# Kernel optimization log

Measured on AMD Instinct MI355X. Metric: run time of the kernel, lower is better.

## Reference

```python
import jax, jax.numpy as jnp
import numpy as np

LOC_SIZE, LOC_EMB = 100000, 256
TIM_SIZE, TIM_EMB = 48, 64
UID_SIZE, UID_EMB = 5000, 128
HID = 512
B, T = 64, 128
L_HIST, G = 1024, 4  # 256 history groups of size 4


def setup_inputs() -> dict:
    key = jax.random.key(0)
    ks = jax.random.split(key, 16)
    s = 0.02
    inp = {
        "loc": jax.random.randint(ks[0], (B, T), 0, LOC_SIZE),
        "tim": jax.random.randint(ks[1], (B, T), 0, TIM_SIZE),
        "input_lengths": jax.random.randint(ks[2], (B,), 1, T + 1),
        "history_loc": jax.random.randint(ks[3], (B, L_HIST), 0, LOC_SIZE),
        "history_tim": jax.random.randint(ks[4], (B, L_HIST), 0, TIM_SIZE),
        "history_uid": jax.random.randint(ks[5], (B, L_HIST), 0, UID_SIZE),
        "group_size": G,
        "emb_loc": jax.random.normal(ks[6], (LOC_SIZE, LOC_EMB), jnp.float32) * s,
        "emb_tim": jax.random.normal(ks[7], (TIM_SIZE, TIM_EMB), jnp.float32) * s,
        "emb_uid": jax.random.normal(ks[8], (UID_SIZE, UID_EMB), jnp.float32) * s,
        "W_attn": jax.random.normal(ks[9], (HID, LOC_EMB + TIM_EMB + UID_EMB), jnp.float32) * s,
        "b_attn": jnp.zeros((HID,), jnp.float32),
        "W_ih": jax.random.normal(ks[10], (3 * HID, LOC_EMB + TIM_EMB), jnp.float32) * s,
        "b_ih": jnp.zeros((3 * HID,), jnp.float32),
        "W_hh": jax.random.normal(ks[11], (3 * HID, HID), jnp.float32) * s,
        "b_hh": jnp.zeros((3 * HID,), jnp.float32),
        "W_final": jax.random.normal(ks[12], (UID_SIZE, 3 * HID), jnp.float32) * s,
        "b_final": jnp.zeros((UID_SIZE,), jnp.float32),
    }
    return inp


def _gru(x_seq, W_ih, b_ih, W_hh, b_hh):
    # x_seq: [T, B, Din] -> outputs [T, B, H], PyTorch gate order (r, z, n)
    H = W_hh.shape[1]
    gx = jnp.einsum("tbd,gd->tbg", x_seq, W_ih) + b_ih  # [T,B,3H]
    h0 = jnp.zeros((x_seq.shape[1], H), x_seq.dtype)

    def step(h, gx_t):
        gh = h @ W_hh.T + b_hh
        xr, xz, xn = jnp.split(gx_t, 3, axis=-1)
        hr, hz, hn = jnp.split(gh, 3, axis=-1)
        r = jax.nn.sigmoid(xr + hr)
        z = jax.nn.sigmoid(xz + hz)
        n = jnp.tanh(xn + r * hn)
        h_new = (1.0 - z) * n + z * h
        return h_new, h_new

    _, outs = jax.lax.scan(step, h0, gx)
    return outs  # [T,B,H]


def reference(loc, tim, input_lengths, history_loc, history_tim, history_uid,
              group_size, emb_loc, emb_tim, emb_uid, W_attn, b_attn,
              W_ih, b_ih, W_hh, b_hh, W_final, b_final):
    Bn, Tn = loc.shape
    # current-trajectory embeddings -> GRU (dropout is identity in eval)
    x = jnp.concatenate([emb_loc[loc], emb_tim[tim]], axis=-1)  # [B,T,Din]
    outs = _gru(jnp.swapaxes(x, 0, 1), W_ih, b_ih, W_hh, b_hh)  # [T,B,H]
    outs = jnp.swapaxes(outs, 0, 1)                              # [B,T,H]
    last = outs[jnp.arange(Bn), input_lengths - 1]               # [B,H]

    # history pooling: groups of size G; uid emb averaged within group,
    # loc/tim embeddings taken at each group's first element
    Gc = group_size
    n_groups = history_uid.shape[1] // Gc
    uid_h = emb_uid[history_uid].reshape(Bn, n_groups, Gc, -1).mean(axis=2)  # [B,N,Du]
    loc_h = emb_loc[history_loc[:, ::Gc]]                                    # [B,N,Dl]
    tim_h = emb_tim[history_tim[:, ::Gc]]                                    # [B,N,Dt]
    hist = jnp.concatenate([loc_h, tim_h, uid_h], axis=-1)
    hist = jnp.tanh(jnp.einsum("bnd,hd->bnh", hist, W_attn) + b_attn)        # [B,N,H]

    # 'dot' attention: replaces the nested python-loop scoring
    energies = jnp.einsum("bh,bnh->bn", last, hist)
    attn_w = jax.nn.softmax(energies, axis=-1)
    context = jnp.einsum("bn,bnh->bh", attn_w, hist)

    out = jnp.concatenate([last, context, last], axis=-1)  # [B,3H]
    y = out @ W_final.T + b_final                          # [B,U]
    # original assigns y (one row) into score[t] of shape [T,U] -> broadcast over T
    score = jnp.broadcast_to(y[:, None, :], (Bn, Tn, y.shape[-1]))
    return score
```

## Files before the change

kernel.cpp:

```cpp
#include <hip/hip_runtime.h>
#include <hip/hip_bf16.h>


typedef __attribute__((ext_vector_type(8))) short bf16x8;
typedef __attribute__((ext_vector_type(4))) float f32x4;
typedef __attribute__((ext_vector_type(4))) unsigned short u16x4;
typedef __attribute__((ext_vector_type(2))) unsigned long long u64x2;
typedef unsigned long long u64;

__device__ inline unsigned short f2bf(float x) {
  __hip_bfloat16 b = __float2bfloat16(x);
  return __builtin_bit_cast(unsigned short, b);
}
__device__ inline bf16x8 pack8(float4 a, float4 b) {
  bf16x8 w;
  w[0]=(short)f2bf(a.x); w[1]=(short)f2bf(a.y); w[2]=(short)f2bf(a.z); w[3]=(short)f2bf(a.w);
  w[4]=(short)f2bf(b.x); w[5]=(short)f2bf(b.y); w[6]=(short)f2bf(b.z); w[7]=(short)f2bf(b.w);
  return w;
}

__global__ __launch_bounds__(256)
void gemm_gx_f(const int* __restrict__ loc, const int* __restrict__ tim,
               const float* __restrict__ eloc, const float* __restrict__ etim,
               const float* __restrict__ W_ih, const float* __restrict__ b_ih,
               float* __restrict__ gx) {
  constexpr int LDR = 40, K = 320, N = 1536;
  __shared__ short Asl[128 * LDR];
  __shared__ short Bsl[128 * LDR];
  const int tid = threadIdx.x;
  const int lane = tid & 63, wid = tid >> 6;
  const int wr = wid >> 1, wc = wid & 1;
  const int m16 = lane & 15, g4 = lane >> 4;
  const int bm = blockIdx.y * 128, bn = blockIdx.x * 128;
  const int srow = tid >> 1, shalf = tid & 1;
  f32x4 acc[4][4] = {};
  for (int k0 = 0; k0 < K; k0 += 32) {
    {
      const int grow = bm + srow;
      const int t = grow >> 6, b = grow & 63;
      const float* ap = (k0 < 256)
        ? eloc + (size_t)loc[b * 128 + t] * 256 + k0 + (shalf << 4)
        : etim + (size_t)tim[b * 128 + t] * 64 + (k0 - 256) + (shalf << 4);
      float4 f0 = ((const float4*)ap)[0], f1 = ((const float4*)ap)[1];
      float4 f2 = ((const float4*)ap)[2], f3 = ((const float4*)ap)[3];
      short* arow = Asl + srow * LDR + (shalf << 4);
      *(bf16x8*)(arow)     = pack8(f0, f1);
      *(bf16x8*)(arow + 8) = pack8(f2, f3);
      const float* bp = W_ih + (size_t)(bn + srow) * K + k0 + (shalf << 4);
      f0 = ((const float4*)bp)[0]; f1 = ((const float4*)bp)[1];
      f2 = ((const float4*)bp)[2]; f3 = ((const float4*)bp)[3];
      short* brow = Bsl + srow * LDR + (shalf << 4);
      *(bf16x8*)(brow)     = pack8(f0, f1);
      *(bf16x8*)(brow + 8) = pack8(f2, f3);
    }
    __syncthreads();
    bf16x8 af[4], bfr[4];
#pragma unroll
    for (int i = 0; i < 4; ++i) {
      af[i]  = *(const bf16x8*)(Asl + ((wr << 6) + (i << 4) + m16) * LDR + (g4 << 3));
      bfr[i] = *(const bf16x8*)(Bsl + ((wc << 6) + (i << 4) + m16) * LDR + (g4 << 3));
    }
#pragma unroll
    for (int i = 0; i < 4; ++i)
#pragma unroll
      for (int j = 0; j < 4; ++j)
        acc[i][j] = __builtin_amdgcn_mfma_f32_16x16x32_bf16(af[i], bfr[j], acc[i][j], 0, 0, 0);
    __syncthreads();
  }
#pragma unroll
  for (int i = 0; i < 4; ++i)
#pragma unroll
    for (int j = 0; j < 4; ++j) {
      const int col = bn + (wc << 6) + (j << 4) + m16;
      const float bv = b_ih[col];
#pragma unroll
      for (int q = 0; q < 4; ++q) {
        const int row = bm + (wr << 6) + (i << 4) + (g4 << 2) + q;
        gx[(size_t)row * N + col] = acc[i][j][q] + bv;
      }
    }
}

__global__ __launch_bounds__(256)
void gru_attn(const float* __restrict__ gx, const float* __restrict__ W_hh,
              const float* __restrict__ b_hh, const int* __restrict__ lens,
              short* __restrict__ h_bf, float* __restrict__ lastb,
              unsigned int* __restrict__ flags,
              const int* __restrict__ hloc, const int* __restrict__ htim,
              const int* __restrict__ huid,
              const float* __restrict__ eloc, const float* __restrict__ etim,
              const float* __restrict__ euid,
              const float* __restrict__ W_attn, const float* __restrict__ b_attn,
              float* __restrict__ histt) {
  __shared__ short smem[6 * 16 * 512];
  const int bid = blockIdx.x;
  const int tid = threadIdx.x;

  if (bid < 64) {
    if (tid >= 128) {
      for (int t = 0; t < 128; ++t) __syncthreads();
      return;
    }
    const int lane = tid & 63, tt = tid >> 6;
    const int c = bid >> 2, grp = bid & 3;
    const int j0 = (c << 5) + (tt << 4);
    const int b0 = grp << 4;
    const int m16 = lane & 15, g4 = lane >> 4;

    for (int gi = 0; gi < 3; ++gi) {
      const float* wg = W_hh + (size_t)(gi * 512 + j0) * 512;
      short* slab = smem + (((gi << 1) + tt) << 13);
      for (int r = 0; r < 16; ++r) {
        int k = lane << 3;
        const float4* src = (const float4*)(wg + (size_t)r * 512 + k);
        int off = ((r << 9) + k) ^ ((r & 7) << 3);
        *(bf16x8*)(slab + off) = pack8(src[0], src[1]);
      }
    }
    __syncthreads();

    const int bcol = b0 + m16;
    const int jr = j0 + (g4 << 2);
    const f32x4 bhr = *(const f32x4*)&b_hh[jr];
    const f32x4 bhz = *(const f32x4*)&b_hh[512 + jr];
    const f32x4 bhn = *(const f32x4*)&b_hh[1024 + jr];
    const int lenb = lens[bcol];
    f32x4 hprev = {0.f, 0.f, 0.f, 0.f};

    unsigned int* gflags = flags + (grp << 8);
    unsigned int* ownflag = gflags + (c << 4);

    for (int t = 0; t < 128; ++t) {
      const float* gxb = gx + ((size_t)t * 64 + bcol) * 1536;
      f32x4 gr = *(const f32x4*)(gxb + jr);
      f32x4 gz = *(const f32x4*)(gxb + 512 + jr);
      f32x4 gn = *(const f32x4*)(gxb + 1024 + jr);
      f32x4 ar = {0.f, 0.f, 0.f, 0.f}, az = ar, an = ar;
      if (t) {
        unsigned tgt = (unsigned)t;
        while (true) {
          unsigned f = tgt;
          if (lane < 16)
            f = __hip_atomic_load(gflags + (lane << 4), __ATOMIC_RELAXED, __HIP_MEMORY_SCOPE_AGENT);
          if (__all((int)(f >= tgt))) break;
        }
        asm volatile("" ::: "memory");

        const u64* hp = (const u64*)(h_bf + ((t & 1) << 15) + (size_t)bcol * 512 + (g4 << 3));
        u64 hu[32];
#pragma unroll
        for (int ks = 0; ks < 16; ++ks) {
          hu[2 * ks]     = __hip_atomic_load(hp + ks * 8,     __ATOMIC_RELAXED, __HIP_MEMORY_SCOPE_AGENT);
          hu[2 * ks + 1] = __hip_atomic_load(hp + ks * 8 + 1, __ATOMIC_RELAXED, __HIP_MEMORY_SCOPE_AGENT);
        }
#define GRU_MFMA(ks)                                                                 \
        {                                                                            \
          u64x2 p; p[0] = hu[2 * (ks)]; p[1] = hu[2 * (ks) + 1];                     \
          bf16x8 hf = __builtin_bit_cast(bf16x8, p);                                 \
          int off = ((m16 << 9) + ((ks) << 5) + (g4 << 3)) ^ ((m16 & 7) << 3);       \
          ar = __builtin_amdgcn_mfma_f32_16x16x32_bf16(*(const bf16x8*)(smem + ((0 + tt) << 13) + off), hf, ar, 0, 0, 0); \
          az = __builtin_amdgcn_mfma_f32_16x16x32_bf16(*(const bf16x8*)(smem + ((2 + tt) << 13) + off), hf, az, 0, 0, 0); \
          an = __builtin_amdgcn_mfma_f32_16x16x32_bf16(*(const bf16x8*)(smem + ((4 + tt) << 13) + off), hf, an, 0, 0, 0); \
        }
        GRU_MFMA(0)  GRU_MFMA(1)  GRU_MFMA(2)  GRU_MFMA(3)
        GRU_MFMA(4)  GRU_MFMA(5)  GRU_MFMA(6)  GRU_MFMA(7)
        GRU_MFMA(8)  GRU_MFMA(9)  GRU_MFMA(10) GRU_MFMA(11)
        GRU_MFMA(12) GRU_MFMA(13) GRU_MFMA(14) GRU_MFMA(15)
#undef GRU_MFMA
      }
      u16x4 hw;
#pragma unroll
      for (int q = 0; q < 4; ++q) {
        float r = 1.f / (1.f + __expf(-(gr[q] + ar[q] + bhr[q])));
        float z = 1.f / (1.f + __expf(-(gz[q] + az[q] + bhz[q])));
        float xn = gn[q] + r * (an[q] + bhn[q]);
        float n = 1.f - 2.f / (__expf(2.f * xn) + 1.f);
        float hv = (1.f - z) * n + z * hprev[q];
        hprev[q] = hv;
        hw[q] = f2bf(hv);
      }
      __hip_atomic_store((u64*)(h_bf + ((~t & 1) << 15) + (size_t)bcol * 512 + jr),
                         __builtin_bit_cast(u64, hw),
                         __ATOMIC_RELAXED, __HIP_MEMORY_SCOPE_AGENT);
      if (t == lenb - 1) {
        *(f32x4*)(lastb + (size_t)bcol * 512 + jr) = hprev;
      }
      if (t < 127) {
        asm volatile("s_waitcnt vmcnt(0)" ::: "memory");
        __syncthreads();
        if (tid == 0)
          __hip_atomic_store(ownflag, (unsigned)(t + 1), __ATOMIC_RELAXED, __HIP_MEMORY_SCOPE_AGENT);
      }
    }
    return;
  }

  constexpr int LDR = 40, K = 448, N = 512;
  short* Asl = smem;
  short* Bsl = smem + 128 * LDR;
  const int lane = tid & 63, wid = tid >> 6;
  const int wr = wid >> 1, wc = wid & 1;
  const int m16 = lane & 15, g4 = lane >> 4;
  const int srow = tid >> 1, shalf = tid & 1;
  for (int tile = bid - 64; tile < 512; tile += 128) {
    const int yt = tile >> 2, nt = tile & 3;
    const int bm = yt << 7, bn = nt << 7;
    f32x4 acc[4][4] = {};
    for (int k0 = 0; k0 < K; k0 += 32) {
      {
        const int grow = bm + srow;
        const int b = grow >> 8, n = grow & 255;
        const int base = b * 1024 + (n << 2);
        float4 f0, f1, f2, f3;
        if (k0 < 256) {
          const float* ap = eloc + (size_t)hloc[base] * 256 + k0 + (shalf << 4);
          f0 = ((const float4*)ap)[0]; f1 = ((const float4*)ap)[1];
          f2 = ((const float4*)ap)[2]; f3 = ((const float4*)ap)[3];
        } else if (k0 < 320) {
          const float* ap = etim + (size_t)htim[base] * 64 + (k0 - 256) + (shalf << 4);
          f0 = ((const float4*)ap)[0]; f1 = ((const float4*)ap)[1];
          f2 = ((const float4*)ap)[2]; f3 = ((const float4*)ap)[3];
        } else {
          const int cu = (k0 - 320) + (shalf << 4);
          const float4* u0 = (const float4*)(euid + (size_t)huid[base + 0] * 128 + cu);
          const float4* u1 = (const float4*)(euid + (size_t)huid[base + 1] * 128 + cu);
          const float4* u2 = (const float4*)(euid + (size_t)huid[base + 2] * 128 + cu);
          const float4* u3 = (const float4*)(euid + (size_t)huid[base + 3] * 128 + cu);
#define AVG4(idx, dst) { float4 a=u0[idx],b4=u1[idx],c4=u2[idx],d4=u3[idx];            \
          dst.x=0.25f*(a.x+b4.x+c4.x+d4.x); dst.y=0.25f*(a.y+b4.y+c4.y+d4.y);         \
          dst.z=0.25f*(a.z+b4.z+c4.z+d4.z); dst.w=0.25f*(a.w+b4.w+c4.w+d4.w); }
          AVG4(0, f0) AVG4(1, f1) AVG4(2, f2) AVG4(3, f3)
#undef AVG4
        }
        short* arow = Asl + srow * LDR + (shalf << 4);
        *(bf16x8*)(arow)     = pack8(f0, f1);
        *(bf16x8*)(arow + 8) = pack8(f2, f3);
        const float* bp = W_attn + (size_t)(bn + srow) * K + k0 + (shalf << 4);
        f0 = ((const float4*)bp)[0]; f1 = ((const float4*)bp)[1];
        f2 = ((const float4*)bp)[2]; f3 = ((const float4*)bp)[3];
        short* brow = Bsl + srow * LDR + (shalf << 4);
        *(bf16x8*)(brow)     = pack8(f0, f1);
        *(bf16x8*)(brow + 8) = pack8(f2, f3);
      }
      __syncthreads();
      bf16x8 af[4], bfr[4];
#pragma unroll
      for (int i = 0; i < 4; ++i) {
        af[i]  = *(const bf16x8*)(Asl + ((wr << 6) + (i << 4) + m16) * LDR + (g4 << 3));
        bfr[i] = *(const bf16x8*)(Bsl + ((wc << 6) + (i << 4) + m16) * LDR + (g4 << 3));
      }
#pragma unroll
      for (int i = 0; i < 4; ++i)
#pragma unroll
        for (int j = 0; j < 4; ++j)
          acc[i][j] = __builtin_amdgcn_mfma_f32_16x16x32_bf16(af[i], bfr[j], acc[i][j], 0, 0, 0);
      __syncthreads();
    }
#pragma unroll
    for (int i = 0; i < 4; ++i)
#pragma unroll
      for (int j = 0; j < 4; ++j) {
        const int col = bn + (wc << 6) + (j << 4) + m16;
        const float bv = b_attn[col];
#pragma unroll
        for (int q = 0; q < 4; ++q) {
          const int row = bm + (wr << 6) + (i << 4) + (g4 << 2) + q;
          histt[(size_t)row * N + col] = tanhf(acc[i][j][q] + bv);
        }
      }
  }
}

__global__ __launch_bounds__(256)
void attn_ctx(const float* __restrict__ histt, const float* __restrict__ last,
              float* __restrict__ ctx) {
  int b = blockIdx.x, tid = threadIdx.x;
  __shared__ float ls[512];
  __shared__ float w[256];
  __shared__ float red[256];
  ((float2*)ls)[tid] = ((const float2*)(last + (size_t)b * 512))[tid];
  __syncthreads();
  const float* hb = histt + (size_t)b * 256 * 512;
  const float* hrow = hb + (size_t)tid * 512;
  float acc = 0.f;
  for (int k = 0; k < 512; k += 4) {
    float4 h4 = *(const float4*)(hrow + k);
    acc += ls[k] * h4.x + ls[k + 1] * h4.y + ls[k + 2] * h4.z + ls[k + 3] * h4.w;
  }
  red[tid] = acc;
  __syncthreads();
  for (int s = 128; s; s >>= 1) {
    if (tid < s) red[tid] = fmaxf(red[tid], red[tid + s]);
    __syncthreads();
  }
  float m = red[0];
  __syncthreads();
  float ex = expf(acc - m);
  w[tid] = ex; red[tid] = ex;
  __syncthreads();
  for (int s = 128; s; s >>= 1) {
    if (tid < s) red[tid] += red[tid + s];
    __syncthreads();
  }
  float inv = 1.f / red[0];
  float c0 = 0.f, c1 = 0.f;
  for (int n = 0; n < 256; ++n) {
    float wn = w[n];
    c0 += wn * hb[(size_t)n * 512 + tid];
    c1 += wn * hb[(size_t)n * 512 + tid + 256];
  }
  ctx[(size_t)b * 512 + tid]       = c0 * inv;
  ctx[(size_t)b * 512 + tid + 256] = c1 * inv;
}

__global__ __launch_bounds__(256)
void final_gemm(const float* __restrict__ last, const float* __restrict__ ctx,
                const float* __restrict__ Wf, const float* __restrict__ bf,
                float* __restrict__ y) {
  __shared__ float s[64][132];
  const int tid = threadIdx.x;
  const int u0 = blockIdx.x << 3;
  const int ul = tid >> 6, b = tid & 63;
  float acc0 = 0.f, acc1 = 0.f;
  for (int kc = 0; kc < 12; ++kc) {
    __syncthreads();
    for (int i = tid; i < 2048; i += 256) {
      int rb = i >> 5, cc = (i & 31) << 2;
      int k = kc * 128 + cc;
      const float* src = (k < 512) ? (last + (size_t)rb * 512 + k)
                       : (k < 1024) ? (ctx + (size_t)rb * 512 + k - 512)
                                    : (last + (size_t)rb * 512 + k - 1024);
      *(float4*)&s[rb][cc] = *(const float4*)src;
    }
    __syncthreads();
#pragma unroll
    for (int uu = 0; uu < 2; ++uu) {
      int u = u0 + ul + uu * 4;
      const float* wrow = Wf + (size_t)u * 1536 + kc * 128;
      float a = 0.f;
#pragma unroll 8
      for (int c = 0; c < 128; c += 4) {
        float4 w4 = *(const float4*)(wrow + c);
        float4 s4 = *(const float4*)&s[b][c];
        a += w4.x * s4.x + w4.y * s4.y + w4.z * s4.z + w4.w * s4.w;
      }
      if (uu == 0) acc0 += a; else acc1 += a;
    }
  }
  int u = u0 + ul;
  y[(size_t)b * 5000 + u]     = acc0 + bf[u];
  y[(size_t)b * 5000 + u + 4] = acc1 + bf[u + 4];
}

__global__ void broadcast_y(const float* __restrict__ y, float* __restrict__ out) {
  int bt = blockIdx.x;
  const float4* src = (const float4*)(y + (size_t)(bt >> 7) * 5000);
  float4* dst = (float4*)(out + (size_t)bt * 5000);
  for (int i = threadIdx.x; i < 1250; i += 256) dst[i] = src[i];
}

extern "C" void kernel_launch(void* const* d_in, const int* in_sizes, int n_in,
                              void* d_out, int out_size, void* d_ws, size_t ws_size,
                              hipStream_t stream) {
  const int* loc  = (const int*)d_in[0];
  const int* tim  = (const int*)d_in[1];
  const int* lens = (const int*)d_in[2];
  const int* hloc = (const int*)d_in[3];
  const int* htim = (const int*)d_in[4];
  const int* huid = (const int*)d_in[5];
  const float* eloc    = (const float*)d_in[7];
  const float* etim    = (const float*)d_in[8];
  const float* euid    = (const float*)d_in[9];
  const float* W_attn  = (const float*)d_in[10];
  const float* b_attn  = (const float*)d_in[11];
  const float* W_ih    = (const float*)d_in[12];
  const float* b_ih    = (const float*)d_in[13];
  const float* W_hh    = (const float*)d_in[14];
  const float* b_hh    = (const float*)d_in[15];
  const float* W_final = (const float*)d_in[16];
  const float* b_final = (const float*)d_in[17];
  float* out = (float*)d_out;
  char* ws = (char*)d_ws;

  float* gx    = (float*)(ws + 0ull);
  float* histt = (float*)(ws + 50331648ull);
  float* lastb = (float*)(ws + 83886080ull);
  float* ctx   = (float*)(ws + 84017152ull);
  float* yv    = (float*)(ws + 84148224ull);
  short* h_bf  = (short*)(ws + 85428224ull);
  unsigned int* flags = (unsigned int*)(ws + 85559296ull);

  hipMemsetAsync(flags, 0, 4096, stream);
  gemm_gx_f<<<dim3(12, 64), 256, 0, stream>>>(loc, tim, eloc, etim, W_ih, b_ih, gx);

  gru_attn<<<192, 256, 0, stream>>>(gx, W_hh, b_hh, lens, h_bf, lastb, flags,
                                    hloc, htim, huid, eloc, etim, euid,
                                    W_attn, b_attn, histt);

  attn_ctx<<<64, 256, 0, stream>>>(histt, lastb, ctx);
  final_gemm<<<625, 256, 0, stream>>>(lastb, ctx, W_final, b_final, yv);
  broadcast_y<<<8192, 256, 0, stream>>>(yv, out);
}
```

Before: 645.6 us.

## Per-wavefront GRU flags, fuse attention context into GRU kernel, prefetch gx GEMM loads

```diff
diff --git a/kernel.cpp b/kernel.cpp
--- a/kernel.cpp
+++ b/kernel.cpp
@@ -33,27 +33,36 @@
   const int m16 = lane & 15, g4 = lane >> 4;
   const int bm = blockIdx.y * 128, bn = blockIdx.x * 128;
   const int srow = tid >> 1, shalf = tid & 1;
+  const int grow = bm + srow;
+  const int t_ = grow >> 6, b_ = grow & 63;
+  const float* aloc = eloc + (size_t)loc[b_ * 128 + t_] * 256 + (shalf << 4);
+  const float* atim = etim + (size_t)tim[b_ * 128 + t_] * 64 + (shalf << 4);
+  const float* bbase = W_ih + (size_t)(bn + srow) * K + (shalf << 4);
+  float4 a0, a1, a2, a3, w0, w1, w2, w3;
+  {
+    a0 = ((const float4*)aloc)[0]; a1 = ((const float4*)aloc)[1];
+    a2 = ((const float4*)aloc)[2]; a3 = ((const float4*)aloc)[3];
+    w0 = ((const float4*)bbase)[0]; w1 = ((const float4*)bbase)[1];
+    w2 = ((const float4*)bbase)[2]; w3 = ((const float4*)bbase)[3];
+  }
   f32x4 acc[4][4] = {};
   for (int k0 = 0; k0 < K; k0 += 32) {
-    {
-      const int grow = bm + srow;
-      const int t = grow >> 6, b = grow & 63;
-      const float* ap = (k0 < 256)
-        ? eloc + (size_t)loc[b * 128 + t] * 256 + k0 + (shalf << 4)
-        : etim + (size_t)tim[b * 128 + t] * 64 + (k0 - 256) + (shalf << 4);
-      float4 f0 = ((const float4*)ap)[0], f1 = ((const float4*)ap)[1];
-      float4 f2 = ((const float4*)ap)[2], f3 = ((const float4*)ap)[3];
-      short* arow = Asl + srow * LDR + (shalf << 4);
-      *(bf16x8*)(arow)     = pack8(f0, f1);
-      *(bf16x8*)(arow + 8) = pack8(f2, f3);
-      const float* bp = W_ih + (size_t)(bn + srow) * K + k0 + (shalf << 4);
-      f0 = ((const float4*)bp)[0]; f1 = ((const float4*)bp)[1];
-      f2 = ((const float4*)bp)[2]; f3 = ((const float4*)bp)[3];
-      short* brow = Bsl + srow * LDR + (shalf << 4);
-      *(bf16x8*)(brow)     = pack8(f0, f1);
-      *(bf16x8*)(brow + 8) = pack8(f2, f3);
-    }
-    __syncthreads();
+    short* arow = Asl + srow * LDR + (shalf << 4);
+    *(bf16x8*)(arow)     = pack8(a0, a1);
+    *(bf16x8*)(arow + 8) = pack8(a2, a3);
+    short* brow = Bsl + srow * LDR + (shalf << 4);
+    *(bf16x8*)(brow)     = pack8(w0, w1);
+    *(bf16x8*)(brow + 8) = pack8(w2, w3);
+    __syncthreads();
+    if (k0 + 32 < K) {
+      const int kn = k0 + 32;
+      const float* ap = (kn < 256) ? (aloc + kn) : (atim + (kn - 256));
+      a0 = ((const float4*)ap)[0]; a1 = ((const float4*)ap)[1];
+      a2 = ((const float4*)ap)[2]; a3 = ((const float4*)ap)[3];
+      const float* bp = bbase + kn;
+      w0 = ((const float4*)bp)[0]; w1 = ((const float4*)bp)[1];
+      w2 = ((const float4*)bp)[2]; w3 = ((const float4*)bp)[3];
+    }
     bf16x8 af[4], bfr[4];
 #pragma unroll
     for (int i = 0; i < 4; ++i) {
@@ -91,16 +100,13 @@
               const float* __restrict__ eloc, const float* __restrict__ etim,
               const float* __restrict__ euid,
               const float* __restrict__ W_attn, const float* __restrict__ b_attn,
-              float* __restrict__ histt) {
+              float* __restrict__ histt, float* __restrict__ ctx) {
   __shared__ short smem[6 * 16 * 512];
   const int bid = blockIdx.x;
   const int tid = threadIdx.x;
 
   if (bid < 64) {
-    if (tid >= 128) {
-      for (int t = 0; t < 128; ++t) __syncthreads();
-      return;
-    }
+    if (tid >= 128) return;
     const int lane = tid & 63, tt = tid >> 6;
     const int c = bid >> 2, grp = bid & 3;
     const int j0 = (c << 5) + (tt << 4);
@@ -117,7 +123,6 @@
         *(bf16x8*)(slab + off) = pack8(src[0], src[1]);
       }
     }
-    __syncthreads();
 
     const int bcol = b0 + m16;
     const int jr = j0 + (g4 << 2);
@@ -127,8 +132,8 @@
     const int lenb = lens[bcol];
     f32x4 hprev = {0.f, 0.f, 0.f, 0.f};
 
-    unsigned int* gflags = flags + (grp << 8);
-    unsigned int* ownflag = gflags + (c << 4);
+    unsigned int* gflags = flags + (grp << 9);
+    unsigned int* ownflag = gflags + (((c << 1) + tt) << 4);
 
     for (int t = 0; t < 128; ++t) {
       const float* gxb = gx + ((size_t)t * 64 + bcol) * 1536;
@@ -140,7 +145,7 @@
         unsigned tgt = (unsigned)t;
         while (true) {
           unsigned f = tgt;
-          if (lane < 16)
+          if (lane < 32)
             f = __hip_atomic_load(gflags + (lane << 4), __ATOMIC_RELAXED, __HIP_MEMORY_SCOPE_AGENT);
           if (__all((int)(f >= tgt))) break;
         }
@@ -187,130 +192,143 @@
       }
       if (t < 127) {
         asm volatile("s_waitcnt vmcnt(0)" ::: "memory");
+        if (lane == 0)
+          __hip_atomic_store(ownflag, (unsigned)(t + 1), __ATOMIC_RELAXED, __HIP_MEMORY_SCOPE_AGENT);
+      }
+    }
+    asm volatile("s_waitcnt vmcnt(0)" ::: "memory");
+    if (lane == 0)
+      __hip_atomic_fetch_add(flags + 2064, 1u, __ATOMIC_RELEASE, __HIP_MEMORY_SCOPE_AGENT);
+    return;
+  }
+
+  {
+    constexpr int LDR = 40, K = 448, N = 512;
+    short* Asl = smem;
+    short* Bsl = smem + 128 * LDR;
+    const int lane = tid & 63, wid = tid >> 6;
+    const int wr = wid >> 1, wc = wid & 1;
+    const int m16 = lane & 15, g4 = lane >> 4;
+    const int srow = tid >> 1, shalf = tid & 1;
+    for (int tile = bid - 64; tile < 512; tile += 128) {
+      const int yt = tile >> 2, nt = tile & 3;
+      const int bm = yt << 7, bn = nt << 7;
+      f32x4 acc[4][4] = {};
+      for (int k0 = 0; k0 < K; k0 += 32) {
+        {
+          const int grow = bm + srow;
+          const int b = grow >> 8, n = grow & 255;
+          const int base = b * 1024 + (n << 2);
+          float4 f0, f1, f2, f3;
+          if (k0 < 256) {
+            const float* ap = eloc + (size_t)hloc[base] * 256 + k0 + (shalf << 4);
+            f0 = ((const float4*)ap)[0]; f1 = ((const float4*)ap)[1];
+            f2 = ((const float4*)ap)[2]; f3 = ((const float4*)ap)[3];
+          } else if (k0 < 320) {
+            const float* ap = etim + (size_t)htim[base] * 64 + (k0 - 256) + (shalf << 4);
+            f0 = ((const float4*)ap)[0]; f1 = ((const float4*)ap)[1];
+            f2 = ((const float4*)ap)[2]; f3 = ((const float4*)ap)[3];
+          } else {
+            const int cu = (k0 - 320) + (shalf << 4);
+            const float4* u0 = (const float4*)(euid + (size_t)huid[base + 0] * 128 + cu);
+            const float4* u1 = (const float4*)(euid + (size_t)huid[base + 1] * 128 + cu);
+            const float4* u2 = (const float4*)(euid + (size_t)huid[base + 2] * 128 + cu);
+            const float4* u3 = (const float4*)(euid + (size_t)huid[base + 3] * 128 + cu);
+#define AVG4(idx, dst) { float4 a=u0[idx],b4=u1[idx],c4=u2[idx],d4=u3[idx];            \
+            dst.x=0.25f*(a.x+b4.x+c4.x+d4.x); dst.y=0.25f*(a.y+b4.y+c4.y+d4.y);       \
+            dst.z=0.25f*(a.z+b4.z+c4.z+d4.z); dst.w=0.25f*(a.w+b4.w+c4.w+d4.w); }
+            AVG4(0, f0) AVG4(1, f1) AVG4(2, f2) AVG4(3, f3)
+#undef AVG4
+          }
+          short* arow = Asl + srow * LDR + (shalf << 4);
+          *(bf16x8*)(arow)     = pack8(f0, f1);
+          *(bf16x8*)(arow + 8) = pack8(f2, f3);
+          const float* bp = W_attn + (size_t)(bn + srow) * K + k0 + (shalf << 4);
+          f0 = ((const float4*)bp)[0]; f1 = ((const float4*)bp)[1];
+          f2 = ((const float4*)bp)[2]; f3 = ((const float4*)bp)[3];
+          short* brow = Bsl + srow * LDR + (shalf << 4);
+          *(bf16x8*)(brow)     = pack8(f0, f1);
+          *(bf16x8*)(brow + 8) = pack8(f2, f3);
+        }
         __syncthreads();
-        if (tid == 0)
-          __hip_atomic_store(ownflag, (unsigned)(t + 1), __ATOMIC_RELAXED, __HIP_MEMORY_SCOPE_AGENT);
-      }
-    }
-    return;
-  }
-
-  constexpr int LDR = 40, K = 448, N = 512;
-  short* Asl = smem;
-  short* Bsl = smem + 128 * LDR;
-  const int lane = tid & 63, wid = tid >> 6;
-  const int wr = wid >> 1, wc = wid & 1;
-  const int m16 = lane & 15, g4 = lane >> 4;
-  const int srow = tid >> 1, shalf = tid & 1;
-  for (int tile = bid - 64; tile < 512; tile += 128) {
-    const int yt = tile >> 2, nt = tile & 3;
-    const int bm = yt << 7, bn = nt << 7;
-    f32x4 acc[4][4] = {};
-    for (int k0 = 0; k0 < K; k0 += 32) {
-      {
-        const int grow = bm + srow;
-        const int b = grow >> 8, n = grow & 255;
-        const int base = b * 1024 + (n << 2);
-        float4 f0, f1, f2, f3;
-        if (k0 < 256) {
-          const float* ap = eloc + (size_t)hloc[base] * 256 + k0 + (shalf << 4);
-          f0 = ((const float4*)ap)[0]; f1 = ((const float4*)ap)[1];
-          f2 = ((const float4*)ap)[2]; f3 = ((const float4*)ap)[3];
-        } else if (k0 < 320) {
-          const float* ap = etim + (size_t)htim[base] * 64 + (k0 - 256) + (shalf << 4);
-          f0 = ((const float4*)ap)[0]; f1 = ((const float4*)ap)[1];
-          f2 = ((const float4*)ap)[2]; f3 = ((const float4*)ap)[3];
-        } else {
-          const int cu = (k0 - 320) + (shalf << 4);
-          const float4* u0 = (const float4*)(euid + (size_t)huid[base + 0] * 128 + cu);
-          const float4* u1 = (const float4*)(euid + (size_t)huid[base + 1] * 128 + cu);
-          const float4* u2 = (const float4*)(euid + (size_t)huid[base + 2] * 128 + cu);
-          const float4* u3 = (const float4*)(euid + (size_t)huid[base + 3] * 128 + cu);
-#define AVG4(idx, dst) { float4 a=u0[idx],b4=u1[idx],c4=u2[idx],d4=u3[idx];            \
-          dst.x=0.25f*(a.x+b4.x+c4.x+d4.x); dst.y=0.25f*(a.y+b4.y+c4.y+d4.y);         \
-          dst.z=0.25f*(a.z+b4.z+c4.z+d4.z); dst.w=0.25f*(a.w+b4.w+c4.w+d4.w); }
-          AVG4(0, f0) AVG4(1, f1) AVG4(2, f2) AVG4(3, f3)
-#undef AVG4
-        }
-        short* arow = Asl + srow * LDR + (shalf << 4);
-        *(bf16x8*)(arow)     = pack8(f0, f1);
-        *(bf16x8*)(arow + 8) = pack8(f2, f3);
-        const float* bp = W_attn + (size_t)(bn + srow) * K + k0 + (shalf << 4);
-        f0 = ((const float4*)bp)[0]; f1 = ((const float4*)bp)[1];
-        f2 = ((const float4*)bp)[2]; f3 = ((const float4*)bp)[3];
-        short* brow = Bsl + srow * LDR + (shalf << 4);
-        *(bf16x8*)(brow)     = pack8(f0, f1);
-        *(bf16x8*)(brow + 8) = pack8(f2, f3);
-      }
+        bf16x8 af[4], bfr[4];
+#pragma unroll
+        for (int i = 0; i < 4; ++i) {
+          af[i]  = *(const bf16x8*)(Asl + ((wr << 6) + (i << 4) + m16) * LDR + (g4 << 3));
+          bfr[i] = *(const bf16x8*)(Bsl + ((wc << 6) + (i << 4) + m16) * LDR + (g4 << 3));
+        }
+#pragma unroll
+        for (int i = 0; i < 4; ++i)
+#pragma unroll
+          for (int j = 0; j < 4; ++j)
+            acc[i][j] = __builtin_amdgcn_mfma_f32_16x16x32_bf16(af[i], bfr[j], acc[i][j], 0, 0, 0);
+        __syncthreads();
+      }
+#pragma unroll
+      for (int i = 0; i < 4; ++i)
+#pragma unroll
+        for (int j = 0; j < 4; ++j) {
+          const int col = bn + (wc << 6) + (j << 4) + m16;
+          const float bv = b_attn[col];
+#pragma unroll
+          for (int q = 0; q < 4; ++q) {
+            const int row = bm + (wr << 6) + (i << 4) + (g4 << 2) + q;
+            histt[(size_t)row * N + col] = tanhf(acc[i][j][q] + bv);
+          }
+        }
+    }
+    asm volatile("s_waitcnt vmcnt(0)" ::: "memory");
+    if (tid == 0)
+      __hip_atomic_fetch_add(flags + 2048, 1u, __ATOMIC_RELEASE, __HIP_MEMORY_SCOPE_AGENT);
+  }
+
+  if (bid < 128) {
+    while (true) {
+      unsigned a = __hip_atomic_load(flags + 2048, __ATOMIC_RELAXED, __HIP_MEMORY_SCOPE_AGENT);
+      unsigned g = __hip_atomic_load(flags + 2064, __ATOMIC_RELAXED, __HIP_MEMORY_SCOPE_AGENT);
+      if (a >= 128u && g >= 128u) break;
+      __builtin_amdgcn_s_sleep(2);
+    }
+    __builtin_amdgcn_fence(__ATOMIC_ACQUIRE, "agent");
+    __syncthreads();
+    const int b = bid - 64;
+    float* ls  = (float*)smem;
+    float* wv  = ls + 512;
+    float* red = wv + 256;
+    ((float2*)ls)[tid] = ((const float2*)(lastb + (size_t)b * 512))[tid];
+    __syncthreads();
+    const float* hb = histt + (size_t)b * 256 * 512;
+    const float* hrow = hb + (size_t)tid * 512;
+    float acc = 0.f;
+    for (int k = 0; k < 512; k += 4) {
+      float4 h4 = *(const float4*)(hrow + k);
+      acc += ls[k] * h4.x + ls[k + 1] * h4.y + ls[k + 2] * h4.z + ls[k + 3] * h4.w;
+    }
+    red[tid] = acc;
+    __syncthreads();
+    for (int s = 128; s; s >>= 1) {
+      if (tid < s) red[tid] = fmaxf(red[tid], red[tid + s]);
       __syncthreads();
-      bf16x8 af[4], bfr[4];
-#pragma unroll
-      for (int i = 0; i < 4; ++i) {
-        af[i]  = *(const bf16x8*)(Asl + ((wr << 6) + (i << 4) + m16) * LDR + (g4 << 3));
-        bfr[i] = *(const bf16x8*)(Bsl + ((wc << 6) + (i << 4) + m16) * LDR + (g4 << 3));
-      }
-#pragma unroll
-      for (int i = 0; i < 4; ++i)
-#pragma unroll
-        for (int j = 0; j < 4; ++j)
-          acc[i][j] = __builtin_amdgcn_mfma_f32_16x16x32_bf16(af[i], bfr[j], acc[i][j], 0, 0, 0);
+    }
+    float m = red[0];
+    __syncthreads();
+    float ex = expf(acc - m);
+    wv[tid] = ex; red[tid] = ex;
+    __syncthreads();
+    for (int s = 128; s; s >>= 1) {
+      if (tid < s) red[tid] += red[tid + s];
       __syncthreads();
     }
-#pragma unroll
-    for (int i = 0; i < 4; ++i)
-#pragma unroll
-      for (int j = 0; j < 4; ++j) {
-        const int col = bn + (wc << 6) + (j << 4) + m16;
-        const float bv = b_attn[col];
-#pragma unroll
-        for (int q = 0; q < 4; ++q) {
-          const int row = bm + (wr << 6) + (i << 4) + (g4 << 2) + q;
-          histt[(size_t)row * N + col] = tanhf(acc[i][j][q] + bv);
-        }
-      }
-  }
-}
-
-__global__ __launch_bounds__(256)
-void attn_ctx(const float* __restrict__ histt, const float* __restrict__ last,
-              float* __restrict__ ctx) {
-  int b = blockIdx.x, tid = threadIdx.x;
-  __shared__ float ls[512];
-  __shared__ float w[256];
-  __shared__ float red[256];
-  ((float2*)ls)[tid] = ((const float2*)(last + (size_t)b * 512))[tid];
-  __syncthreads();
-  const float* hb = histt + (size_t)b * 256 * 512;
-  const float* hrow = hb + (size_t)tid * 512;
-  float acc = 0.f;
-  for (int k = 0; k < 512; k += 4) {
-    float4 h4 = *(const float4*)(hrow + k);
-    acc += ls[k] * h4.x + ls[k + 1] * h4.y + ls[k + 2] * h4.z + ls[k + 3] * h4.w;
-  }
-  red[tid] = acc;
-  __syncthreads();
-  for (int s = 128; s; s >>= 1) {
-    if (tid < s) red[tid] = fmaxf(red[tid], red[tid + s]);
-    __syncthreads();
-  }
-  float m = red[0];
-  __syncthreads();
-  float ex = expf(acc - m);
-  w[tid] = ex; red[tid] = ex;
-  __syncthreads();
-  for (int s = 128; s; s >>= 1) {
-    if (tid < s) red[tid] += red[tid + s];
-    __syncthreads();
-  }
-  float inv = 1.f / red[0];
-  float c0 = 0.f, c1 = 0.f;
-  for (int n = 0; n < 256; ++n) {
-    float wn = w[n];
-    c0 += wn * hb[(size_t)n * 512 + tid];
-    c1 += wn * hb[(size_t)n * 512 + tid + 256];
-  }
-  ctx[(size_t)b * 512 + tid]       = c0 * inv;
-  ctx[(size_t)b * 512 + tid + 256] = c1 * inv;
+    float inv = 1.f / red[0];
+    float c0 = 0.f, c1 = 0.f;
+    for (int n = 0; n < 256; ++n) {
+      float wn = wv[n];
+      c0 += wn * hb[(size_t)n * 512 + tid];
+      c1 += wn * hb[(size_t)n * 512 + tid + 256];
+    }
+    ctx[(size_t)b * 512 + tid]       = c0 * inv;
+    ctx[(size_t)b * 512 + tid + 256] = c1 * inv;
+  }
 }
 
 __global__ __launch_bounds__(256)
@@ -390,14 +408,13 @@
   short* h_bf  = (short*)(ws + 85428224ull);
   unsigned int* flags = (unsigned int*)(ws + 85559296ull);
 
-  hipMemsetAsync(flags, 0, 4096, stream);
+  hipMemsetAsync(flags, 0, 12288, stream);
   gemm_gx_f<<<dim3(12, 64), 256, 0, stream>>>(loc, tim, eloc, etim, W_ih, b_ih, gx);
 
   gru_attn<<<192, 256, 0, stream>>>(gx, W_hh, b_hh, lens, h_bf, lastb, flags,
                                     hloc, htim, huid, eloc, etim, euid,
-                                    W_attn, b_attn, histt);
-
-  attn_ctx<<<64, 256, 0, stream>>>(histt, lastb, ctx);
+                                    W_attn, b_attn, histt, ctx);
+
   final_gemm<<<625, 256, 0, stream>>>(lastb, ctx, W_final, b_final, yv);
   broadcast_y<<<8192, 256, 0, stream>>>(yv, out);
 }
```

Measured after the change: 672.4 us. 4.1% more time.
